# Optimization experiments

Hardware: AMD Instinct MI355X
Metric: run time of the kernel (lower is better)

The kernel has to match this reference:

```python
import jax, jax.numpy as jnp
import numpy as np

B, C, H, W = 4, 32, 64, 64
K = 3
HEADS = 8
SF = 4
D = C * K * K          # 288, unfold token dim
E = D // 2             # 144, reduced dim
DH = E // HEADS        # 18, head dim
SCALE = DH ** -0.5
N = H * W              # 4096 tokens


def unfold(x):
    # x: (B,C,H,W) -> (B, C*K*K, H*W), torch.nn.Unfold ordering (c, kh, kw)
    xp = jnp.pad(x, ((0, 0), (0, 0), (1, 1), (1, 1)))
    patches = jnp.stack([xp[:, :, i:i + H, j:j + W] for i in range(K) for j in range(K)], axis=2)
    return patches.reshape(x.shape[0], C * K * K, H * W)


def fold(cols):
    # inverse of unfold: scatter-add overlapping patches back, crop padding
    b = cols.shape[0]
    y = cols.reshape(b, C, K, K, H, W)
    out = jnp.zeros((b, C, H + 2, W + 2), cols.dtype)
    for i in range(K):
        for j in range(K):
            out = out.at[:, :, i:i + H, j:j + W].add(y[:, :, i, j])
    return out[:, :, 1:-1, 1:-1]


def layernorm_cols(cols, g, b):
    # LayerNorm over D applied on (B,N,D) view, returned as (B,D,N)
    xt = cols.transpose(0, 2, 1)
    mu = xt.mean(-1, keepdims=True)
    var = xt.var(-1, keepdims=True)
    y = (xt - mu) / jnp.sqrt(var + 1e-5) * g + b
    return y.transpose(0, 2, 1)


def emha(x, wr, br, wqkv, we, be):
    # x: (B, D, N)
    b, _, n_tok = x.shape
    xr = jnp.einsum('bdn,ed->ben', x, wr) + br[None, :, None]   # Conv1d k=1 reduction
    t = xr.transpose(0, 2, 1)                                   # (B,N,E)
    qkv = t @ wqkv.T                                            # Linear, no bias
    q, k, v = jnp.split(qkv, 3, axis=-1)
    n = n_tok // SF

    def rs(a):
        return a.reshape(b, n_tok, HEADS, DH).transpose(0, 2, 1, 3).reshape(b, HEADS, SF, n, DH)

    q, k, v = rs(q), rs(k), rs(v)
    attn = jax.nn.softmax(jnp.einsum('bhsnd,bhsmd->bhsnm', q, k) * SCALE, axis=-1)
    o = jnp.einsum('bhsnm,bhsmd->bhsnd', attn, v)
    o = o.reshape(b, HEADS, n_tok, DH).transpose(0, 2, 1, 3).reshape(b, n_tok, E).transpose(0, 2, 1)
    return jnp.einsum('ben,fe->bfn', o, we) + be[None, :, None]  # Conv1d k=1 expansion


def conv3x3(x, w, b):
    y = jax.lax.conv_general_dilated(x, w, (1, 1), ((1, 1), (1, 1)),
                                     dimension_numbers=('NCHW', 'OIHW', 'NCHW'))
    return y + b[None, :, None, None]


def setup_inputs() -> dict:
    key = jax.random.key(0)
    ks = jax.random.split(key, 20)
    s = 0.02
    inp = {
        'x': jax.random.normal(ks[0], (B, C, H, W), jnp.float32),
        'ln_g': jnp.ones((D,), jnp.float32),
        'ln_b': jnp.zeros((D,), jnp.float32),
        'conv_w': jax.random.normal(ks[1], (C, C, 3, 3), jnp.float32) * s,
        'conv_b': jnp.zeros((C,), jnp.float32),
    }
    for i in range(3):
        k0, k1, k2 = jax.random.split(ks[2 + i], 3)
        inp[f'wr{i+1}'] = jax.random.normal(k0, (E, D), jnp.float32) * s
        inp[f'br{i+1}'] = jnp.zeros((E,), jnp.float32)
        inp[f'wqkv{i+1}'] = jax.random.normal(k1, (3 * E, E), jnp.float32) * s
        inp[f'we{i+1}'] = jax.random.normal(k2, (D, E), jnp.float32) * s
        inp[f'be{i+1}'] = jnp.zeros((D,), jnp.float32)
    return inp


def reference(x, ln_g, ln_b, conv_w, conv_b,
              wr1, br1, wqkv1, we1, be1,
              wr2, br2, wqkv2, we2, be2,
              wr3, br3, wqkv3, we3, be3):
    t = x
    for (wr, br, wqkv, we, be) in ((wr1, br1, wqkv1, we1, be1),
                                   (wr2, br2, wqkv2, we2, be2),
                                   (wr3, br3, wqkv3, we3, be3)):
        cols = unfold(t)
        cols_n = layernorm_cols(cols, ln_g, ln_b)
        cols = emha(cols_n, wr, br, wqkv, we, be) + cols
        t = fold(cols)
    return x + jax.nn.elu(conv3x3(t, conv_w, conv_b))
```

## Files before the change

kernel.cpp:

```cpp
#include <hip/hip_runtime.h>
#include <math.h>

#define BN 4
#define CC 32
#define HH 64
#define WW 64
#define DD 288
#define EE 144
#define NTOK 4096
#define SCALE_F 0.2357022603955158f
#define QSCALE  0.3401074286f
#define QKST 384
#define MQKV 528

typedef __bf16 bf16x8 __attribute__((ext_vector_type(8)));
typedef float floatx4 __attribute__((ext_vector_type(4)));
typedef unsigned short u16x8 __attribute__((ext_vector_type(8)));

__device__ __forceinline__ unsigned short f2bf(float x) {
    unsigned int u = __float_as_uint(x);
    u += 0x7fffu + ((u >> 16) & 1u);
    return (unsigned short)(u >> 16);
}
__device__ __forceinline__ float bf2f(unsigned short s) {
    return __uint_as_float(((unsigned int)s) << 16);
}
__device__ __forceinline__ unsigned int pack_bf_trunc(float a, float b) {
    return __builtin_amdgcn_perm(__float_as_uint(b), __float_as_uint(a), 0x07060302u);
}

__global__ __launch_bounds__(256) void setup_k(
    const float* __restrict__ wr0, const float* __restrict__ br0,
    const float* __restrict__ wr1, const float* __restrict__ br1,
    const float* __restrict__ wr2, const float* __restrict__ br2,
    const float* __restrict__ g,  const float* __restrict__ lb,
    const float* __restrict__ wqkv0, const float* __restrict__ wqkv1, const float* __restrict__ wqkv2,
    const float* __restrict__ we0,   const float* __restrict__ we1,   const float* __restrict__ we2,
    unsigned short* __restrict__ wg_bf, float* __restrict__ wgsum, float* __restrict__ wbeta,
    unsigned short* __restrict__ wqkv_bf, unsigned short* __restrict__ we_bf)
{
    int blk = blockIdx.x;
    int tid = threadIdx.x;
    if (blk < 3) {
        if (tid < 144) {
            int l = blk, e = tid;
            const float* wr = (l == 0) ? wr0 : ((l == 1) ? wr1 : wr2);
            const float* br = (l == 0) ? br0 : ((l == 1) ? br1 : br2);
            float sg = 0.f, sb = 0.f;
            for (int d = 0; d < DD; ++d) {
                float w = wr[e * DD + d];
                float wgv = w * g[d];
                wg_bf[((size_t)l * EE + e) * DD + d] = f2bf(wgv);
                sg += wgv;
                sb += w * lb[d];
            }
            wgsum[l * EE + e] = sg;
            wbeta[l * EE + e] = sb + br[e];
        }
        return;
    }
    int idx = (blk - 3) * 256 + tid;
    const int T1 = 3 * MQKV * 160;
    const int T2 = 3 * 288 * 160;
    if (idx < T1) {
        int l = idx / (MQKV * 160), r = idx % (MQKV * 160);
        int m = r / 160, k = r % 160;
        const float* w = (l == 0) ? wqkv0 : ((l == 1) ? wqkv1 : wqkv2);
        float v = 0.f;
        if (k < 144) {
            if (m < 192) {
                int h = m / 24, j = m % 24;
                if (j < 18) v = w[(h * 18 + j) * 144 + k] * QSCALE;
            } else if (m < 384) {
                int mm = m - 192, h = mm / 24, j = mm % 24;
                if (j < 18) v = w[(144 + h * 18 + j) * 144 + k];
            } else {
                v = w[(288 + (m - 384)) * 144 + k];
            }
        }
        wqkv_bf[idx] = f2bf(v);
    } else if (idx < T1 + T2) {
        int j = idx - T1;
        int l = j / (288 * 160), r = j % (288 * 160);
        int m = r / 160, k = r % 160;
        const float* w = (l == 0) ? we0 : ((l == 1) ? we1 : we2);
        we_bf[j] = (k < 144) ? f2bf(w[m * 144 + k]) : 0;
    }
}

__global__ __launch_bounds__(256) void unfold_k(const float* __restrict__ t,
    unsigned short* __restrict__ colsT,
    float* __restrict__ mu, float* __restrict__ rstd)
{
    __shared__ float red1[4][64], red2[4][64];
    int tid = threadIdx.x;
    int lane = tid & 63, cpart = tid >> 6;
    int b = blockIdx.x >> 6, nc = blockIdx.x & 63;
    int n = nc * 64 + lane;
    int h = n >> 6, w = n & 63;
    const float* tb = t + (size_t)b * CC * HH * WW;
    unsigned short loc[72];
    float s1 = 0.f, s2 = 0.f;
    #pragma unroll
    for (int c8 = 0; c8 < 8; ++c8) {
        int c = cpart * 8 + c8;
        const float* tc = tb + (size_t)c * 4096;
        #pragma unroll
        for (int i = 0; i < 3; ++i) {
            int hr = h + i - 1;
            bool rok = ((unsigned)hr < 64u);
            #pragma unroll
            for (int j = 0; j < 3; ++j) {
                int wc = w + j - 1;
                bool ok = rok && ((unsigned)wc < 64u);
                float v = ok ? tc[hr * 64 + wc] : 0.f;
                loc[c8 * 9 + i * 3 + j] = f2bf(v);
                s1 += v;
                s2 = fmaf(v, v, s2);
            }
        }
    }
    unsigned short* ct = colsT + ((size_t)b * NTOK + n) * 288 + cpart * 72;
    #pragma unroll
    for (int u = 0; u < 9; ++u)
        *(u16x8*)&ct[u * 8] = *(const u16x8*)&loc[u * 8];
    red1[cpart][lane] = s1;
    red2[cpart][lane] = s2;
    __syncthreads();
    if (tid < 64) {
        float a = red1[0][tid] + red1[1][tid] + red1[2][tid] + red1[3][tid];
        float q = red2[0][tid] + red2[1][tid] + red2[2][tid] + red2[3][tid];
        float m = a * (1.f / 288.f);
        float var = q * (1.f / 288.f) - m * m;
        int nn = nc * 64 + tid;
        mu[b * NTOK + nn] = m;
        rstd[b * NTOK + nn] = rsqrtf(var + 1e-5f);
    }
}

template<int K, int MODE, int NYB>
__global__ __launch_bounds__(256) void mgemm_k(
    const unsigned short* __restrict__ A, const unsigned short* __restrict__ Bt, int BST,
    unsigned short* __restrict__ Ct, unsigned short* __restrict__ Cv,
    const float* __restrict__ mu, const float* __restrict__ rstd,
    const float* __restrict__ wgsum, const float* __restrict__ wbeta,
    const float* __restrict__ bias)
{
    constexpr int NT = 64;
    __shared__ unsigned short Ts[64 * 56];
    int flat = blockIdx.x;
    int g  = (flat / (8 * NYB)) * 8 + (flat & 7);
    int jm = (flat % (8 * NYB)) >> 3;
    int n0 = (g & 63) * NT;
    int bI = g >> 6;
    int m0 = jm * 48;
    int tid = threadIdx.x;
    int wv = tid >> 6, lane = tid & 63;
    int l15 = lane & 15, l4 = lane >> 4;

    const unsigned short* Arow = A + (size_t)(m0 + l15) * K + l4 * 8;
    const unsigned short* Brow = Bt + ((size_t)bI * NTOK + n0 + wv * 16 + l15) * BST + l4 * 8;

    floatx4 acc[3];
    acc[0] = acc[1] = acc[2] = (floatx4){0.f, 0.f, 0.f, 0.f};

    #pragma unroll
    for (int ks = 0; ks < K / 32; ++ks) {
        bf16x8 bfr = *(const bf16x8*)(Brow + ks * 32);
        #pragma unroll
        for (int mi = 0; mi < 3; ++mi) {
            bf16x8 af = *(const bf16x8*)(Arow + (size_t)mi * 16 * K + ks * 32);
            acc[mi] = __builtin_amdgcn_mfma_f32_16x16x32_bf16(af, bfr, acc[mi], 0, 0, 0);
        }
    }

    int n_l = wv * 16 + l15;

    if (MODE == 2) {
        #pragma unroll
        for (int mi = 0; mi < 3; ++mi)
            #pragma unroll
            for (int r = 0; r < 4; ++r) {
                int m_l = mi * 16 + l4 * 4 + r;
                Ts[m_l * 72 + n_l] = f2bf(acc[mi][r] + bias[m0 + m_l]);
            }
        __syncthreads();
        for (int u = tid; u < 48 * 8; u += 256) {
            int row = u >> 3, seg = u & 7;
            unsigned short* dst = Ct + ((size_t)bI * DD + m0 + row) * NTOK + n0 + seg * 8;
            *(u16x8*)dst = *(const u16x8*)&Ts[row * 72 + seg * 8];
        }
    } else {
        bool vpath = (MODE == 0) && (m0 >= 384);
        float muv = 0.f, rsv = 0.f;
        if (MODE == 1) {
            int n_g = n0 + n_l;
            muv = mu[bI * NTOK + n_g];
            rsv = rstd[bI * NTOK + n_g];
        }
        #pragma unroll
        for (int mi = 0; mi < 3; ++mi)
            #pragma unroll
            for (int r = 0; r < 4; ++r) {
                int m_l = mi * 16 + l4 * 4 + r;
                float v = acc[mi][r];
                if (MODE == 1) v = rsv * (v - muv * wgsum[m0 + m_l]) + wbeta[m0 + m_l];
                if (!vpath) Ts[n_l * 56 + m_l] = f2bf(v);
                else        Ts[m_l * 72 + n_l] = f2bf(v);
            }
        __syncthreads();
        if (!vpath) {
            const int CTS = (MODE == 1) ? 160 : QKST;
            if (tid < 128) {
                int row = tid >> 1, half = tid & 1;
                unsigned short* dst = Ct + ((size_t)bI * NTOK + n0 + row) * CTS + m0 + half * 24;
                const unsigned short* src = &Ts[row * 56 + half * 24];
                #pragma unroll
                for (int u = 0; u < 3; ++u)
                    *(u16x8*)&dst[u * 8] = *(const u16x8*)&src[u * 8];
                if (MODE == 1 && m0 == 96) {
                    u16x8 z = (u16x8)0;
                    *(u16x8*)(Ct + ((size_t)bI * NTOK + n0 + row) * 160 + 144 + half * 8) = z;
                }
            }
        } else {
            for (int u = tid; u < 48 * 8; u += 256) {
                int row = u >> 3, seg = u & 7;
                unsigned short* dst = Cv + ((size_t)bI * EE + (m0 - 384) + row) * NTOK + n0 + seg * 8;
                *(u16x8*)dst = *(const u16x8*)&Ts[row * 72 + seg * 8];
            }
        }
    }
}

__global__ __launch_bounds__(256) void attn_k2(const unsigned short* __restrict__ qkT,
                                               const unsigned short* __restrict__ vF,
                                               unsigned short* __restrict__ oT)
{
    __shared__ unsigned short Ks[128 * 40];
    __shared__ unsigned short Vs[32 * 136];
    __shared__ unsigned short Ps[4 * 32 * 72];

    int blk = blockIdx.x;
    int bhs = blk & 127;
    int qc  = blk >> 7;
    int b = bhs >> 5, h = (bhs >> 2) & 7, s = bhs & 3;
    int tid  = threadIdx.x;
    int wv   = tid >> 6;
    int lane = tid & 63;
    int l15 = lane & 15, l4 = lane >> 4;
    int q0 = qc * 128;
    int tokbase = s * 1024;

    const unsigned short* qkb = qkT + (size_t)b * NTOK * QKST;

    if (tid < 128) {
        u16x8 z = (u16x8)0;
        *(u16x8*)&Ks[tid * 40 + 24] = z;
    } else {
        for (int v = tid - 128; v < 14 * 16; v += 128) {
            int d = 18 + (v >> 4), seg = v & 15;
            unsigned short val = (d == 31) ? (unsigned short)0x3F80 : (unsigned short)0;
            u16x8 vv = (u16x8)val;
            *(u16x8*)&Vs[d * 136 + seg * 8] = vv;
        }
    }

    bf16x8 qf[2];
    #pragma unroll
    for (int ni = 0; ni < 2; ++ni) {
        u16x8 raw = *(const u16x8*)(qkb + (size_t)(tokbase + q0 + wv * 32 + ni * 16 + l15) * QKST
                                    + 24 * h + l4 * 8);
        if (l4 == 3) raw = (u16x8)0;
        qf[ni] = *(bf16x8*)&raw;
    }

    floatx4 oacc[2][2];
    #pragma unroll
    for (int i = 0; i < 2; ++i)
        #pragma unroll
        for (int j = 0; j < 2; ++j)
            oacc[i][j] = (floatx4){0.f, 0.f, 0.f, 0.f};

    unsigned short* Pw = &Ps[wv * 32 * 72];

    u16x8 preg[3];
    int vb = tid - 128;
    bool v3 = (vb < 32);
    if (tid < 128) {
        const unsigned short* src = qkb + (size_t)(tokbase + tid) * QKST + 192 + 24 * h;
        preg[0] = *(const u16x8*)&src[0];
        preg[1] = *(const u16x8*)&src[8];
        preg[2] = *(const u16x8*)&src[16];
    } else {
        const unsigned short* vbb = vF + (size_t)b * EE * NTOK + tokbase;
        #pragma unroll
        for (int u = 0; u < 3; ++u) {
            int idx = vb + u * 128;
            if (u < 2 || v3) {
                int d = idx >> 4, seg = idx & 15;
                preg[u] = *(const u16x8*)(vbb + (size_t)(h * 18 + d) * NTOK + seg * 8);
            }
        }
    }

    for (int c0 = 0; c0 < 1024; c0 += 128) {
        __syncthreads();
        if (tid < 128) {
            unsigned short* dk = &Ks[tid * 40];
            *(u16x8*)&dk[0]  = preg[0];
            *(u16x8*)&dk[8]  = preg[1];
            *(u16x8*)&dk[16] = preg[2];
        } else {
            #pragma unroll
            for (int u = 0; u < 3; ++u) {
                int idx = vb + u * 128;
                if (u < 2 || v3) {
                    int d = idx >> 4, seg = idx & 15;
                    *(u16x8*)&Vs[d * 136 + seg * 8] = preg[u];
                }
            }
        }
        int cn = c0 + 128;
        if (cn < 1024) {
            if (tid < 128) {
                const unsigned short* src = qkb + (size_t)(tokbase + cn + tid) * QKST + 192 + 24 * h;
                preg[0] = *(const u16x8*)&src[0];
                preg[1] = *(const u16x8*)&src[8];
                preg[2] = *(const u16x8*)&src[16];
            } else {
                const unsigned short* vbb = vF + (size_t)b * EE * NTOK + tokbase + cn;
                #pragma unroll
                for (int u = 0; u < 3; ++u) {
                    int idx = vb + u * 128;
                    if (u < 2 || v3) {
                        int d = idx >> 4, seg = idx & 15;
                        preg[u] = *(const u16x8*)(vbb + (size_t)(h * 18 + d) * NTOK + seg * 8);
                    }
                }
            }
        }
        __syncthreads();

        #pragma unroll
        for (int sub = 0; sub < 2; ++sub) {
            bf16x8 kf[4];
            #pragma unroll
            for (int mi = 0; mi < 4; ++mi)
                kf[mi] = *(const bf16x8*)&Ks[(sub * 64 + mi * 16 + l15) * 40 + l4 * 8];

            floatx4 sacc[4][2];
            #pragma unroll
            for (int mi = 0; mi < 4; ++mi)
                #pragma unroll
                for (int ni = 0; ni < 2; ++ni) {
                    floatx4 z = (floatx4){0.f, 0.f, 0.f, 0.f};
                    sacc[mi][ni] = __builtin_amdgcn_mfma_f32_16x16x32_bf16(kf[mi], qf[ni], z, 0, 0, 0);
                }

            #pragma unroll
            for (int mi = 0; mi < 4; ++mi)
                #pragma unroll
                for (int ni = 0; ni < 2; ++ni) {
                    int ql   = ni * 16 + l15;
                    int tokb = mi * 16 + l4 * 4;
                    unsigned int lo = pack_bf_trunc(exp2f(sacc[mi][ni][0]), exp2f(sacc[mi][ni][1]));
                    unsigned int hi = pack_bf_trunc(exp2f(sacc[mi][ni][2]), exp2f(sacc[mi][ni][3]));
                    uint2 pk = make_uint2(lo, hi);
                    *(uint2*)&Pw[ql * 72 + tokb] = pk;
                }

            #pragma unroll
            for (int ks = 0; ks < 2; ++ks) {
                bf16x8 pf[2], vf[2];
                pf[0] = *(const bf16x8*)&Pw[(     l15) * 72 + ks * 32 + l4 * 8];
                pf[1] = *(const bf16x8*)&Pw[(16 + l15) * 72 + ks * 32 + l4 * 8];
                vf[0] = *(const bf16x8*)&Vs[(     l15) * 136 + sub * 64 + ks * 32 + l4 * 8];
                vf[1] = *(const bf16x8*)&Vs[(16 + l15) * 136 + sub * 64 + ks * 32 + l4 * 8];
                #pragma unroll
                for (int mi = 0; mi < 2; ++mi)
                    #pragma unroll
                    for (int nd = 0; nd < 2; ++nd)
                        oacc[mi][nd] = __builtin_amdgcn_mfma_f32_16x16x32_bf16(pf[mi], vf[nd], oacc[mi][nd], 0, 0, 0);
            }
        }
    }

    float* fO = (float*)Pw;
    #pragma unroll
    for (int mi = 0; mi < 2; ++mi)
        #pragma unroll
        for (int r = 0; r < 4; ++r) {
            float lsum = __shfl(oacc[mi][1][r], (lane & 48) | 15, 64);
            float inv  = 1.f / lsum;
            int ql = mi * 16 + l4 * 4 + r;
            fO[ql * 33 + l15] = oacc[mi][0][r] * inv;
            if (l15 < 2) fO[ql * 33 + 16 + l15] = oacc[mi][1][r] * inv;
        }

    {
        int q = lane & 31, dh = lane >> 5;
        size_t rowi = (size_t)b * NTOK + tokbase + q0 + wv * 32 + q;
        unsigned short* orow = oT + rowi * 160 + h * 18;
        for (int i = dh; i < 9; i += 2) {
            float a  = fO[q * 33 + 2 * i];
            float bb = fO[q * 33 + 2 * i + 1];
            *(unsigned int*)&orow[2 * i] = (unsigned)f2bf(a) | ((unsigned)f2bf(bb) << 16);
        }
        if (h == 7) {
            u16x8 z = (u16x8)0;
            *(u16x8*)(oT + rowi * 160 + 144 + dh * 8) = z;
        }
    }
}

__global__ __launch_bounds__(256) void fold_k(const unsigned short* __restrict__ cols,
                                              const float* __restrict__ tprev,
                                              float* __restrict__ t)
{
    int idx = blockIdx.x * 256 + threadIdx.x;
    int w = idx & 63;
    int h = (idx >> 6) & 63;
    int c = (idx >> 12) & 31;
    int b = idx >> 17;
    const unsigned short* cb = cols + (size_t)b * DD * NTOK + (size_t)c * 9 * NTOK;
    float sum = 0.f;
    #pragma unroll
    for (int i = 0; i < 3; ++i) {
        int hs = h + 1 - i;
        if ((unsigned)hs < 64u) {
            #pragma unroll
            for (int j = 0; j < 3; ++j) {
                int ws_ = w + 1 - j;
                if ((unsigned)ws_ < 64u)
                    sum += bf2f(cb[(size_t)(i * 3 + j) * NTOK + hs * 64 + ws_]);
            }
        }
    }
    int ch = (h == 0 || h == 63) ? 2 : 3;
    int cw_ = (w == 0 || w == 63) ? 2 : 3;
    t[idx] = sum + (float)(ch * cw_) * tprev[idx];
}

__global__ __launch_bounds__(256) void conv_k(const float* __restrict__ t,
    const float* __restrict__ cw, const float* __restrict__ cbias,
    const float* __restrict__ x, float* __restrict__ out)
{
    __shared__ float wsh[CC * 9];
    int blk = blockIdx.x;
    int band = blk & 3, co = (blk >> 2) & 31, b = blk >> 7;
    int tid = threadIdx.x;
    for (int u = tid; u < CC * 9; u += 256) wsh[u] = cw[co * CC * 9 + u];
    __syncthreads();
    int h = band * 16 + (tid >> 4);
    int w0 = (tid & 15) << 2;
    const float* tb = t + (size_t)b * CC * 4096;
    float bias = cbias[co];
    float a0 = bias, a1 = bias, a2 = bias, a3 = bias;
    for (int ci = 0; ci < CC; ++ci) {
        const float* tc = tb + (size_t)ci * 4096;
        const float* wr = &wsh[ci * 9];
        #pragma unroll
        for (int i = 0; i < 3; ++i) {
            int hr = h + i - 1;
            if ((unsigned)hr < 64u) {
                const float* row = tc + hr * 64;
                float vl = (w0 > 0)  ? row[w0 - 1] : 0.f;
                float4 c4 = *(const float4*)&row[w0];
                float vr = (w0 < 60) ? row[w0 + 4] : 0.f;
                float wj0 = wr[i * 3], wj1 = wr[i * 3 + 1], wj2 = wr[i * 3 + 2];
                a0 = fmaf(wj0, vl,   a0); a0 = fmaf(wj1, c4.x, a0); a0 = fmaf(wj2, c4.y, a0);
                a1 = fmaf(wj0, c4.x, a1); a1 = fmaf(wj1, c4.y, a1); a1 = fmaf(wj2, c4.z, a1);
                a2 = fmaf(wj0, c4.y, a2); a2 = fmaf(wj1, c4.z, a2); a2 = fmaf(wj2, c4.w, a2);
                a3 = fmaf(wj0, c4.z, a3); a3 = fmaf(wj1, c4.w, a3); a3 = fmaf(wj2, vr,   a3);
            }
        }
    }
    size_t oidx = ((size_t)(b * CC + co) * 4096) + h * 64 + w0;
    float4 xin = *(const float4*)&x[oidx];
    float4 o;
    o.x = xin.x + ((a0 > 0.f) ? a0 : (__expf(a0) - 1.f));
    o.y = xin.y + ((a1 > 0.f) ? a1 : (__expf(a1) - 1.f));
    o.z = xin.z + ((a2 > 0.f) ? a2 : (__expf(a2) - 1.f));
    o.w = xin.w + ((a3 > 0.f) ? a3 : (__expf(a3) - 1.f));
    *(float4*)&out[oidx] = o;
}

extern "C" void kernel_launch(void* const* d_in, const int* in_sizes, int n_in,
                              void* d_out, int out_size, void* d_ws, size_t ws_size,
                              hipStream_t stream)
{
    const float* x    = (const float*)d_in[0];
    const float* ln_g = (const float*)d_in[1];
    const float* ln_b = (const float*)d_in[2];
    const float* cw   = (const float*)d_in[3];
    const float* cb   = (const float*)d_in[4];
    const float* wr[3]   = {(const float*)d_in[5],  (const float*)d_in[10], (const float*)d_in[15]};
    const float* br[3]   = {(const float*)d_in[6],  (const float*)d_in[11], (const float*)d_in[16]};
    const float* wqkv[3] = {(const float*)d_in[7],  (const float*)d_in[12], (const float*)d_in[17]};
    const float* we[3]   = {(const float*)d_in[8],  (const float*)d_in[13], (const float*)d_in[18]};
    const float* be[3]   = {(const float*)d_in[9],  (const float*)d_in[14], (const float*)d_in[19]};
    float* out = (float*)d_out;

    char* p = (char*)d_ws;
    unsigned short* cols_bf = (unsigned short*)p; p += (size_t)BN * DD * NTOK * 2;
    unsigned short* colsT = (unsigned short*)p; p += (size_t)BN * NTOK * 288 * 2;
    unsigned short* oT = colsT;
    unsigned short* xrT   = (unsigned short*)p; p += (size_t)BN * NTOK * 160 * 2;
    unsigned short* qkT   = (unsigned short*)p; p += (size_t)BN * NTOK * QKST * 2;
    unsigned short* vF    = (unsigned short*)p; p += (size_t)BN * EE * NTOK * 2;
    float* mu   = (float*)p;              p += (size_t)BN * NTOK * 4;
    float* rstd = (float*)p;              p += (size_t)BN * NTOK * 4;
    float* tA   = (float*)p;              p += (size_t)BN * CC * HH * WW * 4;
    float* tB   = (float*)p;              p += (size_t)BN * CC * HH * WW * 4;
    unsigned short* wg_bf   = (unsigned short*)p; p += (size_t)3 * EE * DD * 2;
    unsigned short* wqkv_bf = (unsigned short*)p; p += (size_t)3 * MQKV * 160 * 2;
    unsigned short* we_bf   = (unsigned short*)p; p += (size_t)3 * DD * 160 * 2;
    float* wgsum = (float*)p;             p += 3 * EE * 4;
    float* wbeta = (float*)p;             p += 3 * EE * 4;
    (void)in_sizes; (void)n_in; (void)out_size; (void)ws_size;

    setup_k<<<1533, 256, 0, stream>>>(wr[0], br[0], wr[1], br[1], wr[2], br[2], ln_g, ln_b,
                                      wqkv[0], wqkv[1], wqkv[2], we[0], we[1], we[2],
                                      wg_bf, wgsum, wbeta, wqkv_bf, we_bf);

    const float* tin = x;
    float* touts[3] = {tA, tB, tA};
    for (int l = 0; l < 3; ++l) {
        unfold_k<<<256, 256, 0, stream>>>(tin, colsT, mu, rstd);
        mgemm_k<288, 1, 3><<<768, 256, 0, stream>>>(
            wg_bf + (size_t)l * EE * DD, colsT, 288, xrT, nullptr,
            mu, rstd, wgsum + l * EE, wbeta + l * EE, nullptr);
        mgemm_k<160, 0, 11><<<2816, 256, 0, stream>>>(
            wqkv_bf + (size_t)l * MQKV * 160, xrT, 160, qkT, vF,
            nullptr, nullptr, nullptr, nullptr, nullptr);
        attn_k2<<<1024, 256, 0, stream>>>(qkT, vF, oT);
        mgemm_k<160, 2, 6><<<1536, 256, 0, stream>>>(
            we_bf + (size_t)l * DD * 160, oT, 160, cols_bf, nullptr,
            nullptr, nullptr, nullptr, nullptr, be[l]);
        fold_k<<<2048, 256, 0, stream>>>(cols_bf, tin, touts[l]);
        tin = touts[l];
    }
    conv_k<<<512, 256, 0, stream>>>(tA, cw, cb, x, out);
}
```

Measured before the change: 444.8 us.

## Split attention over two key chunks and combine partials in separate kernel

The attention kernel now handles half of each 1024-key segment per block, doubling the grid to 2048 blocks. Each block writes unnormalized fp32 partial outputs plus its row sum to a workspace. A new combine kernel adds the two partials, divides by the summed normalizer and writes the bf16 output. This trades more block parallelism and shorter per-block loops for extra fp32 memory traffic and one more kernel launch per layer.

```diff
diff --git a/kernel.cpp b/kernel.cpp
--- a/kernel.cpp
+++ b/kernel.cpp
@@ -235,7 +235,7 @@
 
 __global__ __launch_bounds__(256) void attn_k2(const unsigned short* __restrict__ qkT,
                                                const unsigned short* __restrict__ vF,
-                                               unsigned short* __restrict__ oT)
+                                               float* __restrict__ part)
 {
     __shared__ unsigned short Ks[128 * 40];
     __shared__ unsigned short Vs[32 * 136];
@@ -243,7 +243,8 @@
 
     int blk = blockIdx.x;
     int bhs = blk & 127;
-    int qc  = blk >> 7;
+    int qc  = (blk >> 7) & 7;
+    int kc  = blk >> 10;
     int b = bhs >> 5, h = (bhs >> 2) & 7, s = bhs & 3;
     int tid  = threadIdx.x;
     int wv   = tid >> 6;
@@ -251,6 +252,7 @@
     int l15 = lane & 15, l4 = lane >> 4;
     int q0 = qc * 128;
     int tokbase = s * 1024;
+    int keybase = tokbase + kc * 512;
 
     const unsigned short* qkb = qkT + (size_t)b * NTOK * QKST;
 
@@ -288,12 +290,12 @@
     int vb = tid - 128;
     bool v3 = (vb < 32);
     if (tid < 128) {
-        const unsigned short* src = qkb + (size_t)(tokbase + tid) * QKST + 192 + 24 * h;
+        const unsigned short* src = qkb + (size_t)(keybase + tid) * QKST + 192 + 24 * h;
         preg[0] = *(const u16x8*)&src[0];
         preg[1] = *(const u16x8*)&src[8];
         preg[2] = *(const u16x8*)&src[16];
     } else {
-        const unsigned short* vbb = vF + (size_t)b * EE * NTOK + tokbase;
+        const unsigned short* vbb = vF + (size_t)b * EE * NTOK + keybase;
         #pragma unroll
         for (int u = 0; u < 3; ++u) {
             int idx = vb + u * 128;
@@ -304,7 +306,7 @@
         }
     }
 
-    for (int c0 = 0; c0 < 1024; c0 += 128) {
+    for (int c0 = 0; c0 < 512; c0 += 128) {
         __syncthreads();
         if (tid < 128) {
             unsigned short* dk = &Ks[tid * 40];
@@ -322,14 +324,14 @@
             }
         }
         int cn = c0 + 128;
-        if (cn < 1024) {
+        if (cn < 512) {
             if (tid < 128) {
-                const unsigned short* src = qkb + (size_t)(tokbase + cn + tid) * QKST + 192 + 24 * h;
+                const unsigned short* src = qkb + (size_t)(keybase + cn + tid) * QKST + 192 + 24 * h;
                 preg[0] = *(const u16x8*)&src[0];
                 preg[1] = *(const u16x8*)&src[8];
                 preg[2] = *(const u16x8*)&src[16];
             } else {
-                const unsigned short* vbb = vF + (size_t)b * EE * NTOK + tokbase + cn;
+                const unsigned short* vbb = vF + (size_t)b * EE * NTOK + keybase + cn;
                 #pragma unroll
                 for (int u = 0; u < 3; ++u) {
                     int idx = vb + u * 128;
@@ -392,26 +394,41 @@
         #pragma unroll
         for (int r = 0; r < 4; ++r) {
             float lsum = __shfl(oacc[mi][1][r], (lane & 48) | 15, 64);
-            float inv  = 1.f / lsum;
             int ql = mi * 16 + l4 * 4 + r;
-            fO[ql * 33 + l15] = oacc[mi][0][r] * inv;
-            if (l15 < 2) fO[ql * 33 + 16 + l15] = oacc[mi][1][r] * inv;
+            fO[ql * 33 + l15] = oacc[mi][0][r];
+            if (l15 < 2) fO[ql * 33 + 16 + l15] = oacc[mi][1][r];
+            if (l15 == 2) fO[ql * 33 + 18] = lsum;
         }
 
     {
         int q = lane & 31, dh = lane >> 5;
         size_t rowi = (size_t)b * NTOK + tokbase + q0 + wv * 32 + q;
-        unsigned short* orow = oT + rowi * 160 + h * 18;
+        float* prow = part + ((size_t)kc * BN * NTOK + rowi) * 160 + h * 18;
         for (int i = dh; i < 9; i += 2) {
-            float a  = fO[q * 33 + 2 * i];
-            float bb = fO[q * 33 + 2 * i + 1];
-            *(unsigned int*)&orow[2 * i] = (unsigned)f2bf(a) | ((unsigned)f2bf(bb) << 16);
-        }
-        if (h == 7) {
-            u16x8 z = (u16x8)0;
-            *(u16x8*)(oT + rowi * 160 + 144 + dh * 8) = z;
-        }
-    }
+            float2 v2 = make_float2(fO[q * 33 + 2 * i], fO[q * 33 + 2 * i + 1]);
+            *(float2*)&prow[2 * i] = v2;
+        }
+        if (dh == 1)
+            part[((size_t)kc * BN * NTOK + rowi) * 160 + 144 + h] = fO[q * 33 + 18];
+    }
+}
+
+__global__ __launch_bounds__(256) void comb_k(const float* __restrict__ p1,
+                                              const float* __restrict__ p2,
+                                              unsigned short* __restrict__ oT)
+{
+    int idx = blockIdx.x * 256 + threadIdx.x;
+    int tok = idx / 160;
+    int e = idx - tok * 160;
+    unsigned short v = 0;
+    if (e < 144) {
+        int h = e / 18;
+        const float* r1 = p1 + (size_t)tok * 160;
+        const float* r2 = p2 + (size_t)tok * 160;
+        float l = r1[144 + h] + r2[144 + h];
+        v = f2bf((r1[e] + r2[e]) / l);
+    }
+    oT[(size_t)tok * 160 + e] = v;
 }
 
 __global__ __launch_bounds__(256) void fold_k(const unsigned short* __restrict__ cols,
@@ -509,6 +526,7 @@
     unsigned short* xrT   = (unsigned short*)p; p += (size_t)BN * NTOK * 160 * 2;
     unsigned short* qkT   = (unsigned short*)p; p += (size_t)BN * NTOK * QKST * 2;
     unsigned short* vF    = (unsigned short*)p; p += (size_t)BN * EE * NTOK * 2;
+    float* part = (float*)p;              p += (size_t)2 * BN * NTOK * 160 * 4;
     float* mu   = (float*)p;              p += (size_t)BN * NTOK * 4;
     float* rstd = (float*)p;              p += (size_t)BN * NTOK * 4;
     float* tA   = (float*)p;              p += (size_t)BN * CC * HH * WW * 4;
@@ -534,7 +552,8 @@
         mgemm_k<160, 0, 11><<<2816, 256, 0, stream>>>(
             wqkv_bf + (size_t)l * MQKV * 160, xrT, 160, qkT, vF,
             nullptr, nullptr, nullptr, nullptr, nullptr);
-        attn_k2<<<1024, 256, 0, stream>>>(qkT, vF, oT);
+        attn_k2<<<2048, 256, 0, stream>>>(qkT, vF, part);
+        comb_k<<<10240, 256, 0, stream>>>(part, part + (size_t)BN * NTOK * 160, oT);
         mgemm_k<160, 2, 6><<<1536, 256, 0, stream>>>(
             we_bf + (size_t)l * DD * 160, oT, 160, cols_bf, nullptr,
             nullptr, nullptr, nullptr, nullptr, be[l]);
```

After: 463.2 us. +4.1%, slower.
